# Kernel optimization log

Measured on AMD Instinct MI355X. Metric: run time of the kernel, lower is better.

## Reference

```python
import jax, jax.numpy as jnp
import numpy as np

B, S, D, H = 4, 2048, 1024, 16
DK = D // H

def setup_inputs() -> dict:
    key = jax.random.key(0)
    ks = jax.random.split(key, 11)
    scale = 1.0 / np.sqrt(D)
    return {
        "query": jax.random.normal(ks[0], (B, S, D), jnp.float32),
        "key_": jax.random.normal(ks[1], (B, S, D), jnp.float32),
        "value": jax.random.normal(ks[2], (B, S, D), jnp.float32),
        "Wq": jax.random.normal(ks[3], (D, D), jnp.float32) * scale,
        "bq": jnp.zeros((D,), jnp.float32),
        "Wk": jax.random.normal(ks[4], (D, D), jnp.float32) * scale,
        "bk": jnp.zeros((D,), jnp.float32),
        "Wv": jax.random.normal(ks[5], (D, D), jnp.float32) * scale,
        "bv": jnp.zeros((D,), jnp.float32),
        "Wo": jax.random.normal(ks[6], (D, D), jnp.float32) * scale,
        "bo": jnp.zeros((D,), jnp.float32),
    }

def reference(query, key_, value, Wq, bq, Wk, bk, Wv, bv, Wo, bo):
    # Linear projections (torch Linear: x @ W.T + b)
    Q = query @ Wq.T + bq            # [B,S,D]
    K = key_ @ Wk.T + bk
    V = value @ Wv.T + bv
    # split heads -> [B,H,S,DK]
    def split(x):
        return x.reshape(B, S, H, DK).transpose(0, 2, 1, 3)
    Qh, Kh, Vh = split(Q), split(K), split(V)
    scores = jnp.einsum("bhqd,bhkd->bhqk", Qh, Kh) / np.sqrt(DK)
    attn = jax.nn.softmax(scores, axis=-1)
    ctx = jnp.einsum("bhqk,bhkd->bhqd", attn, Vh)
    ctx = ctx.transpose(0, 2, 1, 3).reshape(B, S, D)
    return ctx @ Wo.T + bo
```

## Files before the change

### kernel.cpp

```cpp
#include <hip/hip_runtime.h>
#include <hip/hip_bf16.h>
#include <stdint.h>

#define B_ 4
#define S_ 2048
#define D_ 1024
#define H_ 16
#define DK_ 64
#define GM (B_ * S_)
#define GN D_
#define GK D_
#define BM 128
#define BN 128
#define BK 64
#define QBLK 128
#define KVBLK 128
#define LDV 8192

typedef __attribute__((ext_vector_type(8))) __bf16 bf16x8;
typedef __attribute__((ext_vector_type(4))) float f32x4;
typedef __attribute__((ext_vector_type(4))) uint32_t u32x4;
typedef __attribute__((ext_vector_type(2))) uint32_t u32x2;

#if __has_builtin(__builtin_amdgcn_exp2f)
#define EXP2F(x) __builtin_amdgcn_exp2f(x)
#else
#define EXP2F(x) exp2f(x)
#endif

#define SCALE_LOG2E 0.18033688011112042f

__device__ __forceinline__ uint16_t f2bf(float x) {
  uint32_t u = __builtin_bit_cast(uint32_t, x);
  u += 0x7fffu + ((u >> 16) & 1u);
  return (uint16_t)(u >> 16);
}
__device__ __forceinline__ uint32_t cvtpk(float lo, float hi) {
  uint32_t r;
  asm("v_cvt_pk_bf16_f32 %0, %1, %2" : "=v"(r) : "v"(lo), "v"(hi));
  return r;
}
__device__ __forceinline__ void gload_lds16(const void* g, void* l) {
  __builtin_amdgcn_global_load_lds(
      (const __attribute__((address_space(1))) void*)g,
      (__attribute__((address_space(3))) void*)l, 16, 0, 0);
}

struct CvtArgs {
  const float* src[7];
  uint16_t* dst[7];
  int n[7];
  float scale[7];
};

__global__ __launch_bounds__(256) void cvt_f32_bf16(CvtArgs a) {
  const int z = blockIdx.z;
  const float* __restrict__ s = a.src[z];
  uint16_t* __restrict__ d = a.dst[z];
  const float sc = a.scale[z];
  const int nv = a.n[z] >> 3;
  const int stride = gridDim.x * blockDim.x;
  for (int i = blockIdx.x * blockDim.x + threadIdx.x; i < nv; i += stride) {
    f32x4 v0 = *(const f32x4*)(s + (size_t)i * 8);
    f32x4 v1 = *(const f32x4*)(s + (size_t)i * 8 + 4);
    union { uint16_t u[8]; u32x4 q; } o;
#pragma unroll
    for (int j = 0; j < 4; ++j) o.u[j] = f2bf(v0[j] * sc);
#pragma unroll
    for (int j = 0; j < 4; ++j) o.u[4 + j] = f2bf(v1[j] * sc);
    *(u32x4*)(d + (size_t)i * 8) = o.q;
  }
}

struct Gemm3Args {
  const uint16_t* A[3];
  const uint16_t* W[3];
  const float* bias[3];
  float bscale[3];
  void* C[3];
  int ldc[3];
};

template <bool CF32, bool BROW>
__global__ __launch_bounds__(256, 2) void mha_gemm3(Gemm3Args args) {
  const int z = blockIdx.z;
  const char* __restrict__ A = (const char*)args.A[z];
  const char* __restrict__ W = (const char*)args.W[z];
  const float* __restrict__ bias = args.bias[z];
  const float bsc = args.bscale[z];
  void* __restrict__ C = args.C[z];
  const int ldc = args.ldc[z];

  __shared__ alignas(16) uint16_t tA[BM][BK];
  __shared__ alignas(16) uint16_t tW[BN][BK];

  const int tid = threadIdx.x;
  const int lane = tid & 63;
  const int wid = tid >> 6;
  const int wm = wid >> 1, wn = wid & 1;
  const int l16 = lane & 15, g = lane >> 4;

  const int m0 = blockIdx.y * BM;
  const int n0 = blockIdx.x * BN;

  f32x4 acc[4][4] = {};
  const int o = tid * 16;

  for (int k0 = 0; k0 < GK; k0 += BK) {
#pragma unroll
    for (int i = 0; i < 4; ++i) {
      const int oo = o + i * 4096;
      const int row = oo >> 7, colb = oo & 127;
      gload_lds16(A + (size_t)(m0 + row) * (GK * 2) + (size_t)k0 * 2 + colb,
                  ((char*)&tA[0][0]) + i * 4096 + wid * 1024);
      gload_lds16(W + (size_t)(n0 + row) * (GK * 2) + (size_t)k0 * 2 + colb,
                  ((char*)&tW[0][0]) + i * 4096 + wid * 1024);
    }
    __syncthreads();
#pragma unroll
    for (int kk = 0; kk < 2; ++kk) {
      const int kcol = kk * 32 + g * 8;
      bf16x8 af[4], bfr[4];
#pragma unroll
      for (int m = 0; m < 4; ++m)
        af[m] = *(const bf16x8*)&tA[wm * 64 + m * 16 + l16][kcol];
#pragma unroll
      for (int n = 0; n < 4; ++n)
        bfr[n] = *(const bf16x8*)&tW[wn * 64 + n * 16 + l16][kcol];
#pragma unroll
      for (int m = 0; m < 4; ++m)
#pragma unroll
        for (int n = 0; n < 4; ++n)
          acc[m][n] = __builtin_amdgcn_mfma_f32_16x16x32_bf16(
              af[m], bfr[n], acc[m][n], 0, 0, 0);
    }
    __syncthreads();
  }

#pragma unroll
  for (int n = 0; n < 4; ++n) {
    const int col = n0 + wn * 64 + n * 16 + l16;
    const float bvc = BROW ? 0.f : bias[col] * bsc;
#pragma unroll
    for (int m = 0; m < 4; ++m) {
      const int rbase = m0 + wm * 64 + m * 16 + g * 4;
#pragma unroll
      for (int r = 0; r < 4; ++r) {
        const float bv = BROW ? bias[rbase + r] * bsc : bvc;
        const float v = acc[m][n][r] + bv;
        if (CF32)
          ((float*)C)[(size_t)(rbase + r) * ldc + col] = v;
        else
          ((uint16_t*)C)[(size_t)(rbase + r) * ldc + col] = f2bf(v);
      }
    }
  }
}

__global__ __launch_bounds__(256) void mha_attn(
    const uint16_t* __restrict__ Q, const uint16_t* __restrict__ K,
    const uint16_t* __restrict__ Vt, uint16_t* __restrict__ O) {
  __shared__ alignas(16) char K_s[2][16384];
  __shared__ alignas(16) char V_s[2][16384];

  const int tid = threadIdx.x;
  const int lane = tid & 63;
  const int wid = tid >> 6;
  const int l16 = lane & 15, g = lane >> 4;

  const int d = blockIdx.x;
  const int bh = (d & 7) + ((d >> 7) << 3);
  const int qb = (d >> 3) & 15;
  const int b = bh >> 4, h = bh & 15;
  const int q0 = qb * QBLK;

  bf16x8 qf[2][2];
#pragma unroll
  for (int mi = 0; mi < 2; ++mi) {
    const uint16_t* qp = Q + ((size_t)(b * S_) + q0 + mi * 64 + wid * 16 + l16) * D_ +
                         h * DK_ + g * 8;
    qf[mi][0] = *(const bf16x8*)qp;
    qf[mi][1] = *(const bf16x8*)(qp + 32);
  }

  f32x4 o_acc[2][4] = {};
  float lpart[2] = {0.f, 0.f};

  const char* Kb = (const char*)K;
  const char* Vtb = (const char*)Vt;

  int srowK[4], scolK[4], srowV[4], scolV[4];
#pragma unroll
  for (int i = 0; i < 4; ++i) {
    const int oo = tid * 16 + i * 4096;
    srowK[i] = oo >> 7;
    scolK[i] = (oo & 127) ^ ((srowK[i] & 7) << 4);
    srowV[i] = oo >> 8;
    scolV[i] = (oo & 255) ^ ((srowV[i] & 7) << 4);
  }

#define ISSUE_LOADS(buf, kv0)                                                  \
  {                                                                            \
    _Pragma("unroll") for (int i = 0; i < 4; ++i) {                            \
      gload_lds16(Kb + (((size_t)b * S_ + (kv0) + srowK[i]) * D_ + h * DK_) * 2\
                      + scolK[i],                                              \
                  &K_s[buf][0] + i * 4096 + wid * 1024);                       \
      gload_lds16(Vtb + (((size_t)h * DK_ + srowV[i]) * LDV + b * S_ + (kv0))  \
                          * 2 + scolV[i],                                      \
                  &V_s[buf][0] + i * 4096 + wid * 1024);                       \
    }                                                                          \
  }

  ISSUE_LOADS(0, 0);
  __syncthreads();
  int cur = 0;

  const int bsrc = l16 + ((g & 1) << 5);
  const int gsel = g >> 1;

  for (int kv0 = 0; kv0 < S_; kv0 += KVBLK) {
    const bool last = (kv0 + KVBLK >= S_);
    if (!last) ISSUE_LOADS(cur ^ 1, kv0 + KVBLK);

    f32x4 sacc[2][8] = {};
#pragma unroll
    for (int ks = 0; ks < 2; ++ks) {
      const int kcolb = ks * 64 + g * 16;
#pragma unroll
      for (int n = 0; n < 8; ++n) {
        const int kvr = n * 16 + l16;
        const bf16x8 kf =
            *(const bf16x8*)(&K_s[cur][0] + kvr * 128 + (kcolb ^ ((kvr & 7) << 4)));
#pragma unroll
        for (int mi = 0; mi < 2; ++mi)
          sacc[mi][n] = __builtin_amdgcn_mfma_f32_16x16x32_bf16(
              kf, qf[mi][ks], sacc[mi][n], 0, 0, 0);
      }
    }

    uint32_t pb[2][4][4];
#pragma unroll
    for (int mi = 0; mi < 2; ++mi) {
      uint32_t pk0[8][2];
#pragma unroll
      for (int n = 0; n < 8; ++n) {
        float e0 = EXP2F(sacc[mi][n][0]);
        float e1 = EXP2F(sacc[mi][n][1]);
        float e2 = EXP2F(sacc[mi][n][2]);
        float e3 = EXP2F(sacc[mi][n][3]);
        lpart[mi] += (e0 + e1) + (e2 + e3);
        pk0[n][0] = cvtpk(e0, e1);
        pk0[n][1] = cvtpk(e2, e3);
      }
#pragma unroll
      for (int ks = 0; ks < 4; ++ks)
#pragma unroll
        for (int jp = 0; jp < 4; ++jp) {
          const int srcl = bsrc + ((jp >> 1) << 4);
          const uint32_t va = __shfl(pk0[2 * ks][jp & 1], srcl, 64);
          const uint32_t vb = __shfl(pk0[2 * ks + 1][jp & 1], srcl, 64);
          pb[mi][ks][jp] = gsel ? vb : va;
        }
    }

#pragma unroll
    for (int ks = 0; ks < 4; ++ks) {
      const int kcolb = ks * 64 + g * 16;
      bf16x8 pf[2];
#pragma unroll
      for (int mi = 0; mi < 2; ++mi) {
        u32x4 t = {pb[mi][ks][0], pb[mi][ks][1], pb[mi][ks][2], pb[mi][ks][3]};
        pf[mi] = __builtin_bit_cast(bf16x8, t);
      }
#pragma unroll
      for (int n = 0; n < 4; ++n) {
        const int dkr = n * 16 + l16;
        const bf16x8 vf =
            *(const bf16x8*)(&V_s[cur][0] + dkr * 256 + (kcolb ^ ((dkr & 7) << 4)));
#pragma unroll
        for (int mi = 0; mi < 2; ++mi)
          o_acc[mi][n] = __builtin_amdgcn_mfma_f32_16x16x32_bf16(
              vf, pf[mi], o_acc[mi][n], 0, 0, 0);
      }
    }

    if (!last) __syncthreads();
    cur ^= 1;
  }

  float linv[2];
#pragma unroll
  for (int mi = 0; mi < 2; ++mi) {
    float s_ = lpart[mi];
    s_ += __shfl_xor(s_, 16, 64);
    s_ += __shfl_xor(s_, 32, 64);
    linv[mi] = 1.f / s_;
  }
#pragma unroll
  for (int mi = 0; mi < 2; ++mi) {
    const size_t row = (size_t)b * S_ + q0 + mi * 64 + wid * 16 + l16;
    uint16_t* op = O + row * D_ + h * DK_ + g * 4;
#pragma unroll
    for (int n = 0; n < 4; ++n) {
      u32x2 w;
      w[0] = cvtpk(o_acc[mi][n][0] * linv[mi], o_acc[mi][n][1] * linv[mi]);
      w[1] = cvtpk(o_acc[mi][n][2] * linv[mi], o_acc[mi][n][3] * linv[mi]);
      *(u32x2*)(op + n * 16) = w;
    }
  }
}

extern "C" void kernel_launch(void* const* d_in, const int* in_sizes, int n_in,
                              void* d_out, int out_size, void* d_ws,
                              size_t ws_size, hipStream_t stream) {
  (void)in_sizes; (void)n_in; (void)out_size; (void)ws_size;

  const float* query = (const float*)d_in[0];
  const float* key_ = (const float*)d_in[1];
  const float* value = (const float*)d_in[2];
  const float* Wq = (const float*)d_in[3];
  const float* bq = (const float*)d_in[4];
  const float* Wk = (const float*)d_in[5];
  const float* bk = (const float*)d_in[6];
  const float* Wv = (const float*)d_in[7];
  const float* bv = (const float*)d_in[8];
  const float* Wo = (const float*)d_in[9];
  const float* bo = (const float*)d_in[10];

  const size_t nact = (size_t)GM * GN;
  const size_t nw = (size_t)GN * GK;
  uint16_t* p = (uint16_t*)d_ws;
  uint16_t* qb = p; p += nact;
  uint16_t* kb = p; p += nact;
  uint16_t* vb = p; p += nact;
  uint16_t* wq = p; p += nw;
  uint16_t* wk = p; p += nw;
  uint16_t* wv = p; p += nw;
  uint16_t* wo = p; p += nw;
  uint16_t* Qp = p; p += nact;
  uint16_t* Kp = p; p += nact;
  uint16_t* Vt = p; p += nact;
  uint16_t* Cp = p; p += nact;

  CvtArgs ca;
  const float* srcs[7] = {query, key_, value, Wq, Wk, Wv, Wo};
  uint16_t* dsts[7] = {qb, kb, vb, wq, wk, wv, wo};
  const int cnts[7] = {(int)nact, (int)nact, (int)nact, (int)nw,
                       (int)nw,   (int)nw,   (int)nw};
  for (int i = 0; i < 7; ++i) {
    ca.src[i] = srcs[i]; ca.dst[i] = dsts[i]; ca.n[i] = cnts[i];
    ca.scale[i] = 1.0f;
  }
  ca.scale[3] = SCALE_LOG2E;
  cvt_f32_bf16<<<dim3(512, 1, 7), dim3(256), 0, stream>>>(ca);

  Gemm3Args g1;
  g1.A[0] = qb; g1.A[1] = kb; g1.A[2] = kb;
  g1.W[0] = wq; g1.W[1] = wk; g1.W[2] = wk;
  g1.bias[0] = bq; g1.bias[1] = bk; g1.bias[2] = bk;
  g1.bscale[0] = SCALE_LOG2E; g1.bscale[1] = 1.0f; g1.bscale[2] = 1.0f;
  g1.C[0] = Qp; g1.C[1] = Kp; g1.C[2] = Kp;
  g1.ldc[0] = GN; g1.ldc[1] = GN; g1.ldc[2] = GN;
  mha_gemm3<false, false>
      <<<dim3(GN / BN, GM / BM, 2), dim3(256), 0, stream>>>(g1);

  Gemm3Args gv;
  gv.A[0] = wv; gv.W[0] = vb; gv.bias[0] = bv; gv.bscale[0] = 1.0f;
  gv.C[0] = Vt; gv.ldc[0] = LDV;
  gv.A[1] = gv.A[0]; gv.W[1] = gv.W[0]; gv.bias[1] = gv.bias[0];
  gv.bscale[1] = 1.0f; gv.C[1] = gv.C[0]; gv.ldc[1] = LDV;
  gv.A[2] = gv.A[0]; gv.W[2] = gv.W[0]; gv.bias[2] = gv.bias[0];
  gv.bscale[2] = 1.0f; gv.C[2] = gv.C[0]; gv.ldc[2] = LDV;
  mha_gemm3<false, true>
      <<<dim3(GM / BN, GK / BM, 1), dim3(256), 0, stream>>>(gv);

  mha_attn<<<dim3((S_ / QBLK) * B_ * H_), dim3(256), 0, stream>>>(Qp, Kp, Vt, Cp);

  Gemm3Args g2;
  g2.A[0] = Cp; g2.W[0] = wo; g2.bias[0] = bo; g2.C[0] = d_out;
  g2.bscale[0] = 1.0f; g2.ldc[0] = GN;
  g2.A[1] = g2.A[0]; g2.W[1] = g2.W[0]; g2.bias[1] = g2.bias[0];
  g2.C[1] = g2.C[0]; g2.bscale[1] = 1.0f; g2.ldc[1] = GN;
  g2.A[2] = g2.A[0]; g2.W[2] = g2.W[0]; g2.bias[2] = g2.bias[0];
  g2.C[2] = g2.C[0]; g2.bscale[2] = 1.0f; g2.ldc[2] = GN;
  mha_gemm3<true, false>
      <<<dim3(GN / BN, GM / BM, 1), dim3(256), 0, stream>>>(g2);
}
```

Measured before the change: 259.7 us.

## Merge V projection into batched QK GEMM launch and halve attention KV tile

The transposed V projection now runs in the same GEMM launch as Q and K as a third z-slice. Per-slice runtime flags select row bias and swapped block indices, which replaces a separate kernel launch and lets all three projections fill the GPU together. The attention kernel's KV block drops from 128 to 64, which halves shared memory and register use per block to raise occupancy, at the cost of twice as many loop iterations and barriers. The bias branch becomes a runtime check, and the non-swapped bias load for the V slice indexes past the bias array, although the result is not used.

```diff
diff --git a/kernel.cpp b/kernel.cpp
--- a/kernel.cpp
+++ b/kernel.cpp
@@ -14,7 +14,7 @@
 #define BN 128
 #define BK 64
 #define QBLK 128
-#define KVBLK 128
+#define KVBLK 64
 #define LDV 8192
 
 typedef __attribute__((ext_vector_type(8))) __bf16 bf16x8;
@@ -79,9 +79,11 @@
   float bscale[3];
   void* C[3];
   int ldc[3];
+  int brow[3];
+  int swap[3];
 };
 
-template <bool CF32, bool BROW>
+template <bool CF32>
 __global__ __launch_bounds__(256, 2) void mha_gemm3(Gemm3Args args) {
   const int z = blockIdx.z;
   const char* __restrict__ A = (const char*)args.A[z];
@@ -90,6 +92,7 @@
   const float bsc = args.bscale[z];
   void* __restrict__ C = args.C[z];
   const int ldc = args.ldc[z];
+  const int brow = args.brow[z];
 
   __shared__ alignas(16) uint16_t tA[BM][BK];
   __shared__ alignas(16) uint16_t tW[BN][BK];
@@ -100,8 +103,8 @@
   const int wm = wid >> 1, wn = wid & 1;
   const int l16 = lane & 15, g = lane >> 4;
 
-  const int m0 = blockIdx.y * BM;
-  const int n0 = blockIdx.x * BN;
+  const int m0 = (args.swap[z] ? blockIdx.x : blockIdx.y) * BM;
+  const int n0 = (args.swap[z] ? blockIdx.y : blockIdx.x) * BN;
 
   f32x4 acc[4][4] = {};
   const int o = tid * 16;
@@ -140,13 +143,13 @@
 #pragma unroll
   for (int n = 0; n < 4; ++n) {
     const int col = n0 + wn * 64 + n * 16 + l16;
-    const float bvc = BROW ? 0.f : bias[col] * bsc;
+    const float bvc = bias[col] * bsc;
 #pragma unroll
     for (int m = 0; m < 4; ++m) {
       const int rbase = m0 + wm * 64 + m * 16 + g * 4;
 #pragma unroll
       for (int r = 0; r < 4; ++r) {
-        const float bv = BROW ? bias[rbase + r] * bsc : bvc;
+        const float bv = brow ? bias[rbase + r] * bsc : bvc;
         const float v = acc[m][n][r] + bv;
         if (CF32)
           ((float*)C)[(size_t)(rbase + r) * ldc + col] = v;
@@ -160,8 +163,8 @@
 __global__ __launch_bounds__(256) void mha_attn(
     const uint16_t* __restrict__ Q, const uint16_t* __restrict__ K,
     const uint16_t* __restrict__ Vt, uint16_t* __restrict__ O) {
-  __shared__ alignas(16) char K_s[2][16384];
-  __shared__ alignas(16) char V_s[2][16384];
+  __shared__ alignas(16) char K_s[2][8192];
+  __shared__ alignas(16) char V_s[2][8192];
 
   const int tid = threadIdx.x;
   const int lane = tid & 63;
@@ -189,24 +192,22 @@
   const char* Kb = (const char*)K;
   const char* Vtb = (const char*)Vt;
 
-  int srowK[4], scolK[4], srowV[4], scolV[4];
-#pragma unroll
-  for (int i = 0; i < 4; ++i) {
+  int srow[2], scol[2];
+#pragma unroll
+  for (int i = 0; i < 2; ++i) {
     const int oo = tid * 16 + i * 4096;
-    srowK[i] = oo >> 7;
-    scolK[i] = (oo & 127) ^ ((srowK[i] & 7) << 4);
-    srowV[i] = oo >> 8;
-    scolV[i] = (oo & 255) ^ ((srowV[i] & 7) << 4);
+    srow[i] = oo >> 7;
+    scol[i] = (oo & 127) ^ ((srow[i] & 7) << 4);
   }
 
 #define ISSUE_LOADS(buf, kv0)                                                  \
   {                                                                            \
-    _Pragma("unroll") for (int i = 0; i < 4; ++i) {                            \
-      gload_lds16(Kb + (((size_t)b * S_ + (kv0) + srowK[i]) * D_ + h * DK_) * 2\
-                      + scolK[i],                                              \
+    _Pragma("unroll") for (int i = 0; i < 2; ++i) {                            \
+      gload_lds16(Kb + (((size_t)b * S_ + (kv0) + srow[i]) * D_ + h * DK_) * 2 \
+                      + scol[i],                                               \
                   &K_s[buf][0] + i * 4096 + wid * 1024);                       \
-      gload_lds16(Vtb + (((size_t)h * DK_ + srowV[i]) * LDV + b * S_ + (kv0))  \
-                          * 2 + scolV[i],                                      \
+      gload_lds16(Vtb + (((size_t)h * DK_ + srow[i]) * LDV + b * S_ + (kv0))   \
+                          * 2 + scol[i],                                       \
                   &V_s[buf][0] + i * 4096 + wid * 1024);                       \
     }                                                                          \
   }
@@ -222,12 +223,12 @@
     const bool last = (kv0 + KVBLK >= S_);
     if (!last) ISSUE_LOADS(cur ^ 1, kv0 + KVBLK);
 
-    f32x4 sacc[2][8] = {};
+    f32x4 sacc[2][4] = {};
 #pragma unroll
     for (int ks = 0; ks < 2; ++ks) {
       const int kcolb = ks * 64 + g * 16;
 #pragma unroll
-      for (int n = 0; n < 8; ++n) {
+      for (int n = 0; n < 4; ++n) {
         const int kvr = n * 16 + l16;
         const bf16x8 kf =
             *(const bf16x8*)(&K_s[cur][0] + kvr * 128 + (kcolb ^ ((kvr & 7) << 4)));
@@ -238,12 +239,12 @@
       }
     }
 
-    uint32_t pb[2][4][4];
+    uint32_t pb[2][2][4];
 #pragma unroll
     for (int mi = 0; mi < 2; ++mi) {
-      uint32_t pk0[8][2];
-#pragma unroll
-      for (int n = 0; n < 8; ++n) {
+      uint32_t pk0[4][2];
+#pragma unroll
+      for (int n = 0; n < 4; ++n) {
         float e0 = EXP2F(sacc[mi][n][0]);
         float e1 = EXP2F(sacc[mi][n][1]);
         float e2 = EXP2F(sacc[mi][n][2]);
@@ -253,7 +254,7 @@
         pk0[n][1] = cvtpk(e2, e3);
       }
 #pragma unroll
-      for (int ks = 0; ks < 4; ++ks)
+      for (int ks = 0; ks < 2; ++ks)
 #pragma unroll
         for (int jp = 0; jp < 4; ++jp) {
           const int srcl = bsrc + ((jp >> 1) << 4);
@@ -264,7 +265,7 @@
     }
 
 #pragma unroll
-    for (int ks = 0; ks < 4; ++ks) {
+    for (int ks = 0; ks < 2; ++ks) {
       const int kcolb = ks * 64 + g * 16;
       bf16x8 pf[2];
 #pragma unroll
@@ -276,7 +277,7 @@
       for (int n = 0; n < 4; ++n) {
         const int dkr = n * 16 + l16;
         const bf16x8 vf =
-            *(const bf16x8*)(&V_s[cur][0] + dkr * 256 + (kcolb ^ ((dkr & 7) << 4)));
+            *(const bf16x8*)(&V_s[cur][0] + dkr * 128 + (kcolb ^ ((dkr & 7) << 4)));
 #pragma unroll
         for (int mi = 0; mi < 2; ++mi)
           o_acc[mi][n] = __builtin_amdgcn_mfma_f32_16x16x32_bf16(
@@ -355,34 +356,28 @@
   cvt_f32_bf16<<<dim3(512, 1, 7), dim3(256), 0, stream>>>(ca);
 
   Gemm3Args g1;
-  g1.A[0] = qb; g1.A[1] = kb; g1.A[2] = kb;
-  g1.W[0] = wq; g1.W[1] = wk; g1.W[2] = wk;
-  g1.bias[0] = bq; g1.bias[1] = bk; g1.bias[2] = bk;
+  g1.A[0] = qb; g1.A[1] = kb; g1.A[2] = wv;
+  g1.W[0] = wq; g1.W[1] = wk; g1.W[2] = vb;
+  g1.bias[0] = bq; g1.bias[1] = bk; g1.bias[2] = bv;
   g1.bscale[0] = SCALE_LOG2E; g1.bscale[1] = 1.0f; g1.bscale[2] = 1.0f;
-  g1.C[0] = Qp; g1.C[1] = Kp; g1.C[2] = Kp;
-  g1.ldc[0] = GN; g1.ldc[1] = GN; g1.ldc[2] = GN;
-  mha_gemm3<false, false>
-      <<<dim3(GN / BN, GM / BM, 2), dim3(256), 0, stream>>>(g1);
-
-  Gemm3Args gv;
-  gv.A[0] = wv; gv.W[0] = vb; gv.bias[0] = bv; gv.bscale[0] = 1.0f;
-  gv.C[0] = Vt; gv.ldc[0] = LDV;
-  gv.A[1] = gv.A[0]; gv.W[1] = gv.W[0]; gv.bias[1] = gv.bias[0];
-  gv.bscale[1] = 1.0f; gv.C[1] = gv.C[0]; gv.ldc[1] = LDV;
-  gv.A[2] = gv.A[0]; gv.W[2] = gv.W[0]; gv.bias[2] = gv.bias[0];
-  gv.bscale[2] = 1.0f; gv.C[2] = gv.C[0]; gv.ldc[2] = LDV;
-  mha_gemm3<false, true>
-      <<<dim3(GM / BN, GK / BM, 1), dim3(256), 0, stream>>>(gv);
+  g1.C[0] = Qp; g1.C[1] = Kp; g1.C[2] = Vt;
+  g1.ldc[0] = GN; g1.ldc[1] = GN; g1.ldc[2] = LDV;
+  g1.brow[0] = 0; g1.brow[1] = 0; g1.brow[2] = 1;
+  g1.swap[0] = 0; g1.swap[1] = 0; g1.swap[2] = 1;
+  mha_gemm3<false>
+      <<<dim3(GN / BN, GM / BM, 3), dim3(256), 0, stream>>>(g1);
 
   mha_attn<<<dim3((S_ / QBLK) * B_ * H_), dim3(256), 0, stream>>>(Qp, Kp, Vt, Cp);
 
   Gemm3Args g2;
   g2.A[0] = Cp; g2.W[0] = wo; g2.bias[0] = bo; g2.C[0] = d_out;
-  g2.bscale[0] = 1.0f; g2.ldc[0] = GN;
+  g2.bscale[0] = 1.0f; g2.ldc[0] = GN; g2.brow[0] = 0; g2.swap[0] = 0;
   g2.A[1] = g2.A[0]; g2.W[1] = g2.W[0]; g2.bias[1] = g2.bias[0];
   g2.C[1] = g2.C[0]; g2.bscale[1] = 1.0f; g2.ldc[1] = GN;
+  g2.brow[1] = 0; g2.swap[1] = 0;
   g2.A[2] = g2.A[0]; g2.W[2] = g2.W[0]; g2.bias[2] = g2.bias[0];
   g2.C[2] = g2.C[0]; g2.bscale[2] = 1.0f; g2.ldc[2] = GN;
-  mha_gemm3<true, false>
+  g2.brow[2] = 0; g2.swap[2] = 0;
+  mha_gemm3<true>
       <<<dim3(GN / BN, GM / BM, 1), dim3(256), 0, stream>>>(g2);
 }
```

Result: no change. 262.0 us (+0.9%).
